# Optimization experiments

Measured on AMD Instinct MI355X. Metric: run time of the kernel, lower is better.

Reference implementation:

```python
import jax, jax.numpy as jnp
import numpy as np

HIDDEN = 1024
HEADS = 16
HEAD_DIM = HIDDEN // HEADS
FF = 4 * HIDDEN
B, S = 2, 2048


def _linear_params(key, out_dim, in_dim):
    kw, kb = jax.random.split(key)
    bound = 1.0 / np.sqrt(in_dim)
    W = jax.random.uniform(kw, (out_dim, in_dim), jnp.float32, -bound, bound)
    b = jax.random.uniform(kb, (out_dim,), jnp.float32, -bound, bound)
    return W, b


def setup_inputs() -> dict:
    key = jax.random.key(0)
    ks = jax.random.split(key, 8)
    x = jax.random.normal(ks[0], (B, S, HIDDEN), jnp.float32)
    attention_mask = jnp.ones((B, S), jnp.float32)
    Wq, bq = _linear_params(ks[1], HIDDEN, HIDDEN)
    Wk, bk = _linear_params(ks[2], HIDDEN, HIDDEN)
    Wv, bv = _linear_params(ks[3], HIDDEN, HIDDEN)
    Wo, bo = _linear_params(ks[4], HIDDEN, HIDDEN)
    W1, b1 = _linear_params(ks[5], FF, HIDDEN)
    W2, b2 = _linear_params(ks[6], HIDDEN, FF)
    g1 = jnp.ones((HIDDEN,), jnp.float32); be1 = jnp.zeros((HIDDEN,), jnp.float32)
    g2 = jnp.ones((HIDDEN,), jnp.float32); be2 = jnp.zeros((HIDDEN,), jnp.float32)
    return dict(x=x, attention_mask=attention_mask,
                Wq=Wq, bq=bq, Wk=Wk, bk=bk, Wv=Wv, bv=bv, Wo=Wo, bo=bo,
                W1=W1, b1=b1, W2=W2, b2=b2,
                g1=g1, be1=be1, g2=g2, be2=be2)


def _layer_norm(x, g, b, eps=1e-5):
    mu = jnp.mean(x, axis=-1, keepdims=True)
    var = jnp.mean(jnp.square(x - mu), axis=-1, keepdims=True)
    return (x - mu) * jax.lax.rsqrt(var + eps) * g + b


def reference(x, attention_mask, Wq, bq, Wk, bk, Wv, bv, Wo, bo,
              W1, b1, W2, b2, g1, be1, g2, be2):
    # Dropout is identity (eval mode / deterministic reference).
    residual = x
    h = _layer_norm(x, g1, be1)
    # [B,S,H] -> [B,nH,S,dh]
    def heads(t):
        return t.reshape(B, S, HEADS, HEAD_DIM).transpose(0, 2, 1, 3)
    q = heads(h @ Wq.T + bq)
    k = heads(h @ Wk.T + bk)
    v = heads(h @ Wv.T + bv)
    scores = jnp.einsum('bhqd,bhkd->bhqk', q, k) / np.sqrt(HEAD_DIM).astype(np.float32)
    scores = scores + (attention_mask[:, None, None, :] - 1.0) * 10000.0
    attn = jax.nn.softmax(scores, axis=-1)
    ctx = jnp.einsum('bhqk,bhkd->bhqd', attn, v)
    ctx = ctx.transpose(0, 2, 1, 3).reshape(B, S, HIDDEN)
    attn_out = ctx @ Wo.T + bo
    x = residual + attn_out
    residual = x
    h = _layer_norm(x, g2, be2)
    h = jax.nn.gelu(h @ W1.T + b1, approximate=False)
    h = h @ W2.T + b2
    return residual + h
```

## Files before the change

### kernel.cpp

```cpp
#include <hip/hip_runtime.h>
#include <hip/hip_bf16.h>
#include <math.h>

typedef __bf16 bf16;
typedef __bf16 bf16x2 __attribute__((ext_vector_type(2)));
typedef __bf16 bf16x4v __attribute__((ext_vector_type(4)));
typedef __bf16 bf16x8 __attribute__((ext_vector_type(8)));
typedef float  f32x4  __attribute__((ext_vector_type(4)));
typedef unsigned u32x4 __attribute__((ext_vector_type(4)));
typedef unsigned u32x2 __attribute__((ext_vector_type(2)));

#define HIDDEN 1024
#define TOKENS 4096
#define FFDIM  4096
#define SEQ    2048
#define NHEAD  16

#define LOG2E 1.44269504088896340736f

__device__ __forceinline__ void async_copy16(bf16* lds, const bf16* g)
{
    __builtin_amdgcn_global_load_lds(
        (__attribute__((address_space(1))) void*)g,
        (__attribute__((address_space(3))) void*)lds,
        16, 0, 0);
}

__device__ __forceinline__ unsigned pack2(float lo, float hi)
{
    bf16x2 t; t[0] = (bf16)lo; t[1] = (bf16)hi;
    return __builtin_bit_cast(unsigned, t);
}

__device__ __forceinline__ void pl32swap(unsigned& a, unsigned& b)
{
    u32x2 r = __builtin_amdgcn_permlane32_swap(a, b, false, false);
    a = r.x; b = r.y;
}

__global__ __launch_bounds__(256) void cvt_all_kernel(const float* __restrict__ wq,
    const float* __restrict__ wk, const float* __restrict__ wv, const float* __restrict__ wo,
    const float* __restrict__ w1, const float* __restrict__ w2, bf16* __restrict__ out)
{
    size_t i = ((size_t)blockIdx.x * 256 + threadIdx.x) * 4;
    int sel = (int)(i >> 20);
    const float* src;
    size_t off;
    if (sel < 4) { src = (sel == 0) ? wq : (sel == 1) ? wk : (sel == 2) ? wv : wo; off = i & ((1u << 20) - 1); }
    else if (sel < 8) { src = w1; off = i - ((size_t)4 << 20); }
    else              { src = w2; off = i - ((size_t)8 << 20); }
    float4 v = *(const float4*)&src[off];
    bf16x4v o = { (bf16)v.x, (bf16)v.y, (bf16)v.z, (bf16)v.w };
    *(bf16x4v*)&out[i] = o;
}

__global__ __launch_bounds__(256) void concat_bias_kernel(const float* __restrict__ bq,
    const float* __restrict__ bk, const float* __restrict__ bv, float* __restrict__ o)
{
    int i = blockIdx.x * 256 + threadIdx.x;
    float v = (i < 1024) ? bq[i] : (i < 2048 ? bk[i - 1024] : bv[i - 2048]);
    o[i] = v;
}

__global__ __launch_bounds__(256) void ln_kernel(const float* __restrict__ in,
    const float* __restrict__ g, const float* __restrict__ be, bf16* __restrict__ out)
{
    int row = blockIdx.x;
    int tid = threadIdx.x;
    const float* x = in + (size_t)row * HIDDEN;
    int i0 = tid * 4;
    float4 v = *(const float4*)&x[i0];
    float s  = v.x + v.y + v.z + v.w;
    float s2 = v.x*v.x + v.y*v.y + v.z*v.z + v.w*v.w;
    #pragma unroll
    for (int off = 32; off > 0; off >>= 1) { s += __shfl_xor(s, off); s2 += __shfl_xor(s2, off); }
    __shared__ float red[2][4];
    int wave = tid >> 6;
    if ((tid & 63) == 0) { red[0][wave] = s; red[1][wave] = s2; }
    __syncthreads();
    float ts  = red[0][0] + red[0][1] + red[0][2] + red[0][3];
    float ts2 = red[1][0] + red[1][1] + red[1][2] + red[1][3];
    float mu   = ts  * (1.0f / HIDDEN);
    float var  = ts2 * (1.0f / HIDDEN) - mu * mu;
    float rstd = rsqrtf(var + 1e-5f);
    float4 gg = *(const float4*)&g[i0];
    float4 bb = *(const float4*)&be[i0];
    bf16x4v o;
    o[0] = (bf16)((v.x - mu) * rstd * gg.x + bb.x);
    o[1] = (bf16)((v.y - mu) * rstd * gg.y + bb.y);
    o[2] = (bf16)((v.z - mu) * rstd * gg.z + bb.z);
    o[3] = (bf16)((v.w - mu) * rstd * gg.w + bb.w);
    *(bf16x4v*)&out[(size_t)row * HIDDEN + i0] = o;
}

template<int BM, int EPI, typename OT>
__global__ __launch_bounds__(256) void gemm_bt(const bf16* __restrict__ A, const bf16* __restrict__ Bt,
    const float* __restrict__ bias, const float* __restrict__ res, OT* __restrict__ C,
    int M, int N, int K)
{
    constexpr int MT = BM / 32;
    __shared__ bf16 As[BM * 64];
    __shared__ bf16 Bs[128 * 64];
    int tid  = threadIdx.x;
    int wave = tid >> 6, lane = tid & 63;
    int lm = lane & 15, quad = lane >> 4;
    int m0 = blockIdx.x * BM, n0 = blockIdx.y * 128;
    int wm = (wave >> 1) * (MT * 16), wn = (wave & 1) * 64;
    int r8 = lane >> 3, c8 = lane & 7;
    int gsw = (c8 ^ (r8 & 7)) * 8;
    f32x4 acc[MT][4] = {};
    for (int k0 = 0; k0 < K; k0 += 64) {
        #pragma unroll
        for (int ch = wave; ch < BM / 8; ch += 4)
            async_copy16(As + ch * 512, &A[(size_t)(m0 + ch * 8 + r8) * K + k0 + gsw]);
        #pragma unroll
        for (int ch = wave; ch < 16; ch += 4)
            async_copy16(Bs + ch * 512, &Bt[(size_t)(n0 + ch * 8 + r8) * K + k0 + gsw]);
        __syncthreads();
        bf16x8 af[MT][2], bfr[4][2];
        #pragma unroll
        for (int ks = 0; ks < 2; ks++) {
            int co = ((ks * 4 + quad) ^ (lm & 7)) * 8;
            #pragma unroll
            for (int t = 0; t < MT; t++) af[t][ks]  = *(const bf16x8*)&As[(wm + t * 16 + lm) * 64 + co];
            #pragma unroll
            for (int t = 0; t < 4; t++)  bfr[t][ks] = *(const bf16x8*)&Bs[(wn + t * 16 + lm) * 64 + co];
        }
        #pragma unroll
        for (int mt = 0; mt < MT; mt++)
            #pragma unroll
            for (int nt = 0; nt < 4; nt++)
                #pragma unroll
                for (int ks = 0; ks < 2; ks++)
                    acc[mt][nt] = __builtin_amdgcn_mfma_f32_16x16x32_bf16(af[mt][ks], bfr[nt][ks], acc[mt][nt], 0, 0, 0);
        __syncthreads();
    }
    #pragma unroll
    for (int mt = 0; mt < MT; mt++) {
        #pragma unroll
        for (int nt = 0; nt < 4; nt++) {
            int col = n0 + wn + nt * 16 + lm;
            float bv = bias[col];
            #pragma unroll
            for (int r = 0; r < 4; r++) {
                int row = m0 + wm + mt * 16 + quad * 4 + r;
                float vv = acc[mt][nt][r] + bv;
                if (EPI == 1) vv = 0.5f * vv * (1.0f + erff(vv * 0.70710678118654752f));
                if (EPI == 2) vv += res[(size_t)row * N + col];
                C[(size_t)row * N + col] = (OT)vv;
            }
        }
    }
}

__global__ __launch_bounds__(256) void gemm_qkv(const bf16* __restrict__ A, const bf16* __restrict__ W,
    const float* __restrict__ bias, bf16* __restrict__ qb, bf16* __restrict__ kb, bf16* __restrict__ vt)
{
    constexpr int K = HIDDEN;
    __shared__ bf16 As[128 * 64];
    __shared__ bf16 Bs[128 * 64];
    int tid  = threadIdx.x;
    int wave = tid >> 6, lane = tid & 63;
    int lm = lane & 15, quad = lane >> 4;
    int m0 = blockIdx.x * 128, n0 = blockIdx.y * 128;
    int wm = (wave >> 1) * 64, wn = (wave & 1) * 64;
    int r8 = lane >> 3, c8 = lane & 7;
    int gsw = (c8 ^ (r8 & 7)) * 8;
    f32x4 acc[4][4] = {};
    for (int k0 = 0; k0 < K; k0 += 64) {
        #pragma unroll
        for (int ch = wave; ch < 16; ch += 4) {
            async_copy16(As + ch * 512, &A[(size_t)(m0 + ch * 8 + r8) * K + k0 + gsw]);
            async_copy16(Bs + ch * 512, &W[(size_t)(n0 + ch * 8 + r8) * K + k0 + gsw]);
        }
        __syncthreads();
        bf16x8 af[4][2], bfr[4][2];
        #pragma unroll
        for (int ks = 0; ks < 2; ks++) {
            int co = ((ks * 4 + quad) ^ (lm & 7)) * 8;
            #pragma unroll
            for (int t = 0; t < 4; t++) {
                af[t][ks]  = *(const bf16x8*)&As[(wm + t * 16 + lm) * 64 + co];
                bfr[t][ks] = *(const bf16x8*)&Bs[(wn + t * 16 + lm) * 64 + co];
            }
        }
        #pragma unroll
        for (int mt = 0; mt < 4; mt++)
            #pragma unroll
            for (int nt = 0; nt < 4; nt++)
                #pragma unroll
                for (int ks = 0; ks < 2; ks++)
                    acc[mt][nt] = __builtin_amdgcn_mfma_f32_16x16x32_bf16(af[mt][ks], bfr[nt][ks], acc[mt][nt], 0, 0, 0);
        __syncthreads();
    }
    int region = n0 >> 10;
    #pragma unroll
    for (int mt = 0; mt < 4; mt++) {
        #pragma unroll
        for (int nt = 0; nt < 4; nt++) {
            int col = n0 + wn + nt * 16 + lm;
            float bv = bias[col];
            int cl = col & 1023;
            #pragma unroll
            for (int r = 0; r < 4; r++) {
                int row = m0 + wm + mt * 16 + quad * 4 + r;
                float vv = acc[mt][nt][r] + bv;
                if (region == 0)      qb[(size_t)row * HIDDEN + cl] = (bf16)vv;
                else if (region == 1) kb[(size_t)row * HIDDEN + cl] = (bf16)vv;
                else {
                    int h = cl >> 6, d = cl & 63;
                    int b = row >> 11, s = row & 2047;
                    vt[(((size_t)(b * NHEAD + h)) * 64 + d) * SEQ + s] = (bf16)vv;
                }
            }
        }
    }
}

__global__ __launch_bounds__(512, 4) void attn_kernel(const bf16* __restrict__ Q, const bf16* __restrict__ K,
    const bf16* __restrict__ Vt, const float* __restrict__ mask, bf16* __restrict__ O)
{
    __shared__ bf16 smem[16384];
    bf16* Ks0 = smem;
    bf16* Ks1 = smem + 4096;
    bf16* Vs0 = smem + 8192;
    bf16* Vs1 = smem + 12288;
    int tid = threadIdx.x, wave = tid >> 6, lane = tid & 63;
    int lm = lane & 15, quad = lane >> 4;
    int pair = wave >> 1, h = wave & 1;
    int bh = blockIdx.y, b = bh >> 4;
    int q0 = blockIdx.x * 128 + pair * 32;
    const size_t base  = ((size_t)b * SEQ) * HIDDEN + (bh & 15) * 64;
    const size_t vbase = (size_t)bh * 64 * SEQ;
    int srow8 = lane >> 3, spos = lane & 7;
    bf16x8 qf[2][2];
    #pragma unroll
    for (int qt = 0; qt < 2; qt++)
        #pragma unroll
        for (int ks = 0; ks < 2; ks++)
            qf[qt][ks] = *(const bf16x8*)&Q[base + (size_t)(q0 + qt * 16 + lm) * HIDDEN + ks * 32 + quad * 8];
    bf16x8 onesf;
    #pragma unroll
    for (int i = 0; i < 8; i++) onesf[i] = (bf16)1.0f;
    f32x4 o[2][4] = {};
    f32x4 lacc[2] = {};
    const float c0 = 0.125f * LOG2E;
    const float cmk = 10000.0f * LOG2E;
    const float coff = -(cmk + 16.0f);
    int r = wave * 8 + srow8;
    int gc = spos ^ (r & 7);
    auto stage = [&](bf16* kd, bf16* vd, int kt) {
        async_copy16(kd + wave * 512, &K [base  + (size_t)(kt + r) * HIDDEN + gc * 8]);
        async_copy16(vd + wave * 512, &Vt[vbase + (size_t)r * SEQ + kt + gc * 8]);
    };
    stage(Ks0, Vs0, 0);
    int kh = h * 32;
    bool qodd = (quad & 1);
    for (int ti = 0; ti < SEQ / 64; ti++) {
        __syncthreads();
        const bf16* ksb = (ti & 1) ? Ks1 : Ks0;
        const bf16* vsb = (ti & 1) ? Vs1 : Vs0;
        if (ti + 1 < SEQ / 64) {
            if (ti & 1) stage(Ks0, Vs0, (ti + 1) * 64);
            else        stage(Ks1, Vs1, (ti + 1) * 64);
        }
        int kt = ti * 64;
        bf16x8 kf[2][2];
        #pragma unroll
        for (int nt = 0; nt < 2; nt++)
            #pragma unroll
            for (int ks = 0; ks < 2; ks++)
                kf[nt][ks] = *(const bf16x8*)&ksb[(kh + nt * 16 + lm) * 64 + (((ks * 4 + quad) ^ (lm & 7)) * 8)];
        f32x4 st[2][2] = {};
        #pragma unroll
        for (int qt = 0; qt < 2; qt++)
            #pragma unroll
            for (int nt = 0; nt < 2; nt++)
                #pragma unroll
                for (int ks = 0; ks < 2; ks++)
                    st[qt][nt] = __builtin_amdgcn_mfma_f32_16x16x32_bf16(kf[nt][ks], qf[qt][ks], st[qt][nt], 0, 0, 0);
        float madd[2][4];
        #pragma unroll
        for (int nt = 0; nt < 2; nt++) {
            float4 mv = *(const float4*)&mask[b * SEQ + kt + kh + nt * 16 + quad * 4];
            madd[nt][0] = mv.x * cmk + coff; madd[nt][1] = mv.y * cmk + coff;
            madd[nt][2] = mv.z * cmk + coff; madd[nt][3] = mv.w * cmk + coff;
        }
        bf16x8 af[2];
        #pragma unroll
        for (int qt = 0; qt < 2; qt++) {
            unsigned w[2][2];
            #pragma unroll
            for (int nt = 0; nt < 2; nt++) {
                float p0 = __builtin_amdgcn_exp2f(st[qt][nt][0] * c0 + madd[nt][0]);
                float p1 = __builtin_amdgcn_exp2f(st[qt][nt][1] * c0 + madd[nt][1]);
                float p2 = __builtin_amdgcn_exp2f(st[qt][nt][2] * c0 + madd[nt][2]);
                float p3 = __builtin_amdgcn_exp2f(st[qt][nt][3] * c0 + madd[nt][3]);
                w[nt][0] = pack2(p0, p1);
                w[nt][1] = pack2(p2, p3);
            }
            unsigned A0 = w[0][0], B0 = w[1][0];
            unsigned A1 = w[0][1], B1 = w[1][1];
            pl32swap(A0, B0);
            pl32swap(A1, B1);
            unsigned F0 = __shfl_xor(A0, 16), G0 = __shfl_xor(B0, 16);
            unsigned F1 = __shfl_xor(A1, 16), G1 = __shfl_xor(B1, 16);
            u32x4 uu;
            uu.x = qodd ? G0 : A0;
            uu.y = qodd ? G1 : A1;
            uu.z = qodd ? B0 : F0;
            uu.w = qodd ? B1 : F1;
            af[qt] = __builtin_bit_cast(bf16x8, uu);
            lacc[qt] = __builtin_amdgcn_mfma_f32_16x16x32_bf16(af[qt], onesf, lacc[qt], 0, 0, 0);
        }
        #pragma unroll
        for (int dt = 0; dt < 4; dt++) {
            bf16x8 vf = *(const bf16x8*)&vsb[(dt * 16 + lm) * 64 + (((4 * h + quad) ^ (lm & 7)) * 8)];
            #pragma unroll
            for (int qt = 0; qt < 2; qt++)
                o[qt][dt] = __builtin_amdgcn_mfma_f32_16x16x32_bf16(af[qt], vf, o[qt][dt], 0, 0, 0);
        }
    }
    __syncthreads();
    float* scratch = (float*)smem;
    float* s = scratch + ((size_t)pair * 64 + lane) * 20;
    if (h == 1) {
        #pragma unroll
        for (int dt = 0; dt < 4; dt++) *(f32x4*)&s[dt * 4] = o[0][dt];
        *(f32x4*)&s[16] = lacc[0];
    }
    __syncthreads();
    if (h == 0) {
        f32x4 pl = *(const f32x4*)&s[16];
        #pragma unroll
        for (int rr = 0; rr < 4; rr++) {
            float inv = 1.0f / (lacc[0][rr] + pl[rr]);
            #pragma unroll
            for (int dt = 0; dt < 4; dt++) {
                float val = (o[0][dt][rr] + s[dt * 4 + rr]) * inv;
                O[base + (size_t)(q0 + quad * 4 + rr) * HIDDEN + dt * 16 + lm] = (bf16)val;
            }
        }
    }
    __syncthreads();
    if (h == 0) {
        #pragma unroll
        for (int dt = 0; dt < 4; dt++) *(f32x4*)&s[dt * 4] = o[1][dt];
        *(f32x4*)&s[16] = lacc[1];
    }
    __syncthreads();
    if (h == 1) {
        f32x4 pl = *(const f32x4*)&s[16];
        #pragma unroll
        for (int rr = 0; rr < 4; rr++) {
            float inv = 1.0f / (lacc[1][rr] + pl[rr]);
            #pragma unroll
            for (int dt = 0; dt < 4; dt++) {
                float val = (o[1][dt][rr] + s[dt * 4 + rr]) * inv;
                O[base + (size_t)(q0 + 16 + quad * 4 + rr) * HIDDEN + dt * 16 + lm] = (bf16)val;
            }
        }
    }
}

extern "C" void kernel_launch(void* const* d_in, const int* in_sizes, int n_in,
                              void* d_out, int out_size, void* d_ws, size_t ws_size,
                              hipStream_t stream)
{
    (void)in_sizes; (void)n_in; (void)out_size; (void)ws_size;
    const float* x    = (const float*)d_in[0];
    const float* mask = (const float*)d_in[1];
    const float* Wq   = (const float*)d_in[2];
    const float* bq   = (const float*)d_in[3];
    const float* Wk   = (const float*)d_in[4];
    const float* bk   = (const float*)d_in[5];
    const float* Wv   = (const float*)d_in[6];
    const float* bv   = (const float*)d_in[7];
    const float* Wo   = (const float*)d_in[8];
    const float* bo   = (const float*)d_in[9];
    const float* W1   = (const float*)d_in[10];
    const float* b1   = (const float*)d_in[11];
    const float* W2   = (const float*)d_in[12];
    const float* b2   = (const float*)d_in[13];
    const float* g1   = (const float*)d_in[14];
    const float* be1  = (const float*)d_in[15];
    const float* g2   = (const float*)d_in[16];
    const float* be2  = (const float*)d_in[17];
    float* out = (float*)d_out;

    const size_t M1 = 1024u * 1024u;
    bf16* ws    = (bf16*)d_ws;
    bf16* Wqkv_b = ws;
    bf16* Wo_b  = ws + 3 * M1;
    bf16* W1_b  = ws + 4 * M1;
    bf16* W2_b  = ws + 8 * M1;
    bf16* qb    = ws + 12 * M1;
    bf16* kb    = ws + 16 * M1;
    bf16* vt    = ws + 20 * M1;
    bf16* cx    = ws + 24 * M1;
    bf16* h     = ws + 28 * M1;
    bf16* ffb   = ws + 12 * M1;
    float* biasqkv = (float*)(ws + 24 * M1);

    cvt_all_kernel<<<dim3(12288), 256, 0, stream>>>(Wq, Wk, Wv, Wo, W1, W2, Wqkv_b);
    concat_bias_kernel<<<dim3(12), 256, 0, stream>>>(bq, bk, bv, biasqkv);

    ln_kernel<<<dim3(TOKENS), 256, 0, stream>>>(x, g1, be1, h);
    gemm_qkv<<<dim3(32, 24), 256, 0, stream>>>(h, Wqkv_b, biasqkv, qb, kb, vt);
    attn_kernel<<<dim3(SEQ / 128, 32), 512, 0, stream>>>(qb, kb, vt, mask, cx);
    gemm_bt<64, 2, float><<<dim3(64, 8), 256, 0, stream>>>(cx, Wo_b, bo, x, out, TOKENS, HIDDEN, HIDDEN);
    ln_kernel<<<dim3(TOKENS), 256, 0, stream>>>(out, g2, be2, h);
    gemm_bt<128, 1, bf16><<<dim3(32, 32), 256, 0, stream>>>(h, W1_b, b1, nullptr, ffb, TOKENS, FFDIM, HIDDEN);
    gemm_bt<64, 2, float><<<dim3(64, 8), 256, 0, stream>>>(ffb, W2_b, b2, out, out, TOKENS, HIDDEN, FFDIM);
}
```

Measured before the change: 370.9 us.

## Double attention K/V stage size per barrier and use fast erf polynomial in GELU

The attention kernel now stages two 64-key tiles per double-buffer slot, growing LDS to 64KB, and processes 128 keys per barrier. This halves the number of __syncthreads and async-copy issue points. The FFN1 GELU epilogue swaps erff for an Abramowitz-Stegun polynomial using rcp and exp2 intrinsics, which cuts epilogue ALU cost but adds approximation error of roughly 1e-7. The larger LDS footprint may reduce attention occupancy below the declared 4 blocks per CU.

```diff
diff --git a/kernel.cpp b/kernel.cpp
--- a/kernel.cpp
+++ b/kernel.cpp
@@ -36,6 +36,17 @@
 {
     u32x2 r = __builtin_amdgcn_permlane32_swap(a, b, false, false);
     a = r.x; b = r.y;
+}
+
+__device__ __forceinline__ float gelu_fast(float v)
+{
+    float x = fabsf(v) * 0.70710678118654752f;
+    float t = __builtin_amdgcn_rcpf(1.0f + 0.3275911f * x);
+    float p = t * (0.254829592f + t * (-0.284496736f + t * (1.421413741f + t * (-1.453152027f + t * 1.061405429f))));
+    float e = __builtin_amdgcn_exp2f(-x * x * LOG2E);
+    float erfv = 1.0f - p * e;
+    erfv = (v < 0.0f) ? -erfv : erfv;
+    return 0.5f * v * (1.0f + erfv);
 }
 
 __global__ __launch_bounds__(256) void cvt_all_kernel(const float* __restrict__ wq,
@@ -145,7 +156,7 @@
             for (int r = 0; r < 4; r++) {
                 int row = m0 + wm + mt * 16 + quad * 4 + r;
                 float vv = acc[mt][nt][r] + bv;
-                if (EPI == 1) vv = 0.5f * vv * (1.0f + erff(vv * 0.70710678118654752f));
+                if (EPI == 1) vv = gelu_fast(vv);
                 if (EPI == 2) vv += res[(size_t)row * N + col];
                 C[(size_t)row * N + col] = (OT)vv;
             }
@@ -220,11 +231,7 @@
 __global__ __launch_bounds__(512, 4) void attn_kernel(const bf16* __restrict__ Q, const bf16* __restrict__ K,
     const bf16* __restrict__ Vt, const float* __restrict__ mask, bf16* __restrict__ O)
 {
-    __shared__ bf16 smem[16384];
-    bf16* Ks0 = smem;
-    bf16* Ks1 = smem + 4096;
-    bf16* Vs0 = smem + 8192;
-    bf16* Vs1 = smem + 12288;
+    __shared__ bf16 smem[32768];
     int tid = threadIdx.x, wave = tid >> 6, lane = tid & 63;
     int lm = lane & 15, quad = lane >> 4;
     int pair = wave >> 1, h = wave & 1;
@@ -249,76 +256,82 @@
     const float coff = -(cmk + 16.0f);
     int r = wave * 8 + srow8;
     int gc = spos ^ (r & 7);
-    auto stage = [&](bf16* kd, bf16* vd, int kt) {
-        async_copy16(kd + wave * 512, &K [base  + (size_t)(kt + r) * HIDDEN + gc * 8]);
-        async_copy16(vd + wave * 512, &Vt[vbase + (size_t)r * SEQ + kt + gc * 8]);
+    auto stage = [&](int gbuf, int ktg) {
+        #pragma unroll
+        for (int s = 0; s < 2; s++) {
+            bf16* kd = smem + ((gbuf << 1) + s) * 4096;
+            bf16* vd = smem + 16384 + ((gbuf << 1) + s) * 4096;
+            int kt = ktg + s * 64;
+            async_copy16(kd + wave * 512, &K [base  + (size_t)(kt + r) * HIDDEN + gc * 8]);
+            async_copy16(vd + wave * 512, &Vt[vbase + (size_t)r * SEQ + kt + gc * 8]);
+        }
     };
-    stage(Ks0, Vs0, 0);
+    stage(0, 0);
     int kh = h * 32;
     bool qodd = (quad & 1);
-    for (int ti = 0; ti < SEQ / 64; ti++) {
+    for (int gi = 0; gi < SEQ / 128; gi++) {
         __syncthreads();
-        const bf16* ksb = (ti & 1) ? Ks1 : Ks0;
-        const bf16* vsb = (ti & 1) ? Vs1 : Vs0;
-        if (ti + 1 < SEQ / 64) {
-            if (ti & 1) stage(Ks0, Vs0, (ti + 1) * 64);
-            else        stage(Ks1, Vs1, (ti + 1) * 64);
-        }
-        int kt = ti * 64;
-        bf16x8 kf[2][2];
-        #pragma unroll
-        for (int nt = 0; nt < 2; nt++)
-            #pragma unroll
-            for (int ks = 0; ks < 2; ks++)
-                kf[nt][ks] = *(const bf16x8*)&ksb[(kh + nt * 16 + lm) * 64 + (((ks * 4 + quad) ^ (lm & 7)) * 8)];
-        f32x4 st[2][2] = {};
-        #pragma unroll
-        for (int qt = 0; qt < 2; qt++)
+        if (gi + 1 < SEQ / 128) stage((gi + 1) & 1, (gi + 1) * 128);
+        #pragma unroll
+        for (int sub = 0; sub < 2; sub++) {
+            const bf16* ksb = smem + (((gi & 1) << 1) + sub) * 4096;
+            const bf16* vsb = smem + 16384 + (((gi & 1) << 1) + sub) * 4096;
+            int kt = gi * 128 + sub * 64;
+            bf16x8 kf[2][2];
             #pragma unroll
             for (int nt = 0; nt < 2; nt++)
                 #pragma unroll
                 for (int ks = 0; ks < 2; ks++)
-                    st[qt][nt] = __builtin_amdgcn_mfma_f32_16x16x32_bf16(kf[nt][ks], qf[qt][ks], st[qt][nt], 0, 0, 0);
-        float madd[2][4];
-        #pragma unroll
-        for (int nt = 0; nt < 2; nt++) {
-            float4 mv = *(const float4*)&mask[b * SEQ + kt + kh + nt * 16 + quad * 4];
-            madd[nt][0] = mv.x * cmk + coff; madd[nt][1] = mv.y * cmk + coff;
-            madd[nt][2] = mv.z * cmk + coff; madd[nt][3] = mv.w * cmk + coff;
-        }
-        bf16x8 af[2];
-        #pragma unroll
-        for (int qt = 0; qt < 2; qt++) {
-            unsigned w[2][2];
+                    kf[nt][ks] = *(const bf16x8*)&ksb[(kh + nt * 16 + lm) * 64 + (((ks * 4 + quad) ^ (lm & 7)) * 8)];
+            f32x4 st[2][2] = {};
+            #pragma unroll
+            for (int qt = 0; qt < 2; qt++)
+                #pragma unroll
+                for (int nt = 0; nt < 2; nt++)
+                    #pragma unroll
+                    for (int ks = 0; ks < 2; ks++)
+                        st[qt][nt] = __builtin_amdgcn_mfma_f32_16x16x32_bf16(kf[nt][ks], qf[qt][ks], st[qt][nt], 0, 0, 0);
+            float madd[2][4];
             #pragma unroll
             for (int nt = 0; nt < 2; nt++) {
-                float p0 = __builtin_amdgcn_exp2f(st[qt][nt][0] * c0 + madd[nt][0]);
-                float p1 = __builtin_amdgcn_exp2f(st[qt][nt][1] * c0 + madd[nt][1]);
-                float p2 = __builtin_amdgcn_exp2f(st[qt][nt][2] * c0 + madd[nt][2]);
-                float p3 = __builtin_amdgcn_exp2f(st[qt][nt][3] * c0 + madd[nt][3]);
-                w[nt][0] = pack2(p0, p1);
-                w[nt][1] = pack2(p2, p3);
-            }
-            unsigned A0 = w[0][0], B0 = w[1][0];
-            unsigned A1 = w[0][1], B1 = w[1][1];
-            pl32swap(A0, B0);
-            pl32swap(A1, B1);
-            unsigned F0 = __shfl_xor(A0, 16), G0 = __shfl_xor(B0, 16);
-            unsigned F1 = __shfl_xor(A1, 16), G1 = __shfl_xor(B1, 16);
-            u32x4 uu;
-            uu.x = qodd ? G0 : A0;
-            uu.y = qodd ? G1 : A1;
-            uu.z = qodd ? B0 : F0;
-            uu.w = qodd ? B1 : F1;
-            af[qt] = __builtin_bit_cast(bf16x8, uu);
-            lacc[qt] = __builtin_amdgcn_mfma_f32_16x16x32_bf16(af[qt], onesf, lacc[qt], 0, 0, 0);
-        }
-        #pragma unroll
-        for (int dt = 0; dt < 4; dt++) {
-            bf16x8 vf = *(const bf16x8*)&vsb[(dt * 16 + lm) * 64 + (((4 * h + quad) ^ (lm & 7)) * 8)];
-            #pragma unroll
-            for (int qt = 0; qt < 2; qt++)
-                o[qt][dt] = __builtin_amdgcn_mfma_f32_16x16x32_bf16(af[qt], vf, o[qt][dt], 0, 0, 0);
+                float4 mv = *(const float4*)&mask[b * SEQ + kt + kh + nt * 16 + quad * 4];
+                madd[nt][0] = mv.x * cmk + coff; madd[nt][1] = mv.y * cmk + coff;
+                madd[nt][2] = mv.z * cmk + coff; madd[nt][3] = mv.w * cmk + coff;
+            }
+            bf16x8 af[2];
+            #pragma unroll
+            for (int qt = 0; qt < 2; qt++) {
+                unsigned w[2][2];
+                #pragma unroll
+                for (int nt = 0; nt < 2; nt++) {
+                    float p0 = __builtin_amdgcn_exp2f(st[qt][nt][0] * c0 + madd[nt][0]);
+                    float p1 = __builtin_amdgcn_exp2f(st[qt][nt][1] * c0 + madd[nt][1]);
+                    float p2 = __builtin_amdgcn_exp2f(st[qt][nt][2] * c0 + madd[nt][2]);
+                    float p3 = __builtin_amdgcn_exp2f(st[qt][nt][3] * c0 + madd[nt][3]);
+                    w[nt][0] = pack2(p0, p1);
+                    w[nt][1] = pack2(p2, p3);
+                }
+                unsigned A0 = w[0][0], B0 = w[1][0];
+                unsigned A1 = w[0][1], B1 = w[1][1];
+                pl32swap(A0, B0);
+                pl32swap(A1, B1);
+                unsigned F0 = __shfl_xor(A0, 16), G0 = __shfl_xor(B0, 16);
+                unsigned F1 = __shfl_xor(A1, 16), G1 = __shfl_xor(B1, 16);
+                u32x4 uu;
+                uu.x = qodd ? G0 : A0;
+                uu.y = qodd ? G1 : A1;
+                uu.z = qodd ? B0 : F0;
+                uu.w = qodd ? B1 : F1;
+                af[qt] = __builtin_bit_cast(bf16x8, uu);
+                lacc[qt] = __builtin_amdgcn_mfma_f32_16x16x32_bf16(af[qt], onesf, lacc[qt], 0, 0, 0);
+            }
+            #pragma unroll
+            for (int dt = 0; dt < 4; dt++) {
+                bf16x8 vf = *(const bf16x8*)&vsb[(dt * 16 + lm) * 64 + (((4 * h + quad) ^ (lm & 7)) * 8)];
+                #pragma unroll
+                for (int qt = 0; qt < 2; qt++)
+                    o[qt][dt] = __builtin_amdgcn_mfma_f32_16x16x32_bf16(af[qt], vf, o[qt][dt], 0, 0, 0);
+            }
         }
     }
     __syncthreads();
```

Measured after the change: 371.3 us. Within noise of the previous version (+0.1%).
